# Kernel optimization log

Hardware: AMD Instinct MI355X
Metric: run time of the kernel (lower is better)

## Reference

```python
import jax, jax.numpy as jnp
import numpy as np

B, T, D, H, C = 128, 512, 128, 64, 45

def _p(key, shape, scale):
    return jax.random.normal(key, shape, dtype=jnp.float32) * scale

def setup_inputs() -> dict:
    key = jax.random.key(0)
    ks = jax.random.split(key, 10)
    sD, sH, s2H = 1.0 / np.sqrt(D), 1.0 / np.sqrt(H), 1.0 / np.sqrt(2 * H)
    b = jnp.zeros((4 * H,), jnp.float32)
    return {
        "x": jax.random.normal(ks[0], (B, T, D), dtype=jnp.float32),
        "W1f": _p(ks[1], (D, 4 * H), sD), "U1f": _p(ks[2], (H, 4 * H), sH), "b1f": b,
        "W1b": _p(ks[3], (D, 4 * H), sD), "U1b": _p(ks[4], (H, 4 * H), sH), "b1b": b,
        "W2f": _p(ks[5], (2 * H, 4 * H), s2H), "U2f": _p(ks[6], (H, 4 * H), sH), "b2f": b,
        "W2b": _p(ks[7], (2 * H, 4 * H), s2H), "U2b": _p(ks[8], (H, 4 * H), sH), "b2b": b,
        "Wd": _p(ks[9], (2 * H, C), s2H), "bd": jnp.zeros((C,), jnp.float32),
    }

def _lstm_dir(x, W, U, b, reverse):
    # Keras LSTM with activation=relu, recurrent_activation=sigmoid, gate order [i,f,c,o].
    if reverse:
        x = x[:, ::-1, :]
    xz = jnp.einsum('btd,dg->btg', x, W) + b  # precompute input projections [B,T,4H]
    h0 = jnp.zeros((x.shape[0], H), x.dtype)

    def step(carry, z_t):
        h, c = carry
        z = z_t + h @ U  # [B,4H]
        i, f, g, o = jnp.split(z, 4, axis=-1)
        c = jax.nn.sigmoid(f) * c + jax.nn.sigmoid(i) * jax.nn.relu(g)
        h = jax.nn.sigmoid(o) * jax.nn.relu(c)
        return (h, c), h

    _, hs = jax.lax.scan(step, (h0, h0), jnp.swapaxes(xz, 0, 1))  # [T,B,H]
    hs = jnp.swapaxes(hs, 0, 1)  # [B,T,H]
    return hs[:, ::-1, :] if reverse else hs

def reference(x, W1f, U1f, b1f, W1b, U1b, b1b, W2f, U2f, b2f, W2b, U2b, b2b, Wd, bd):
    h1 = jnp.concatenate([_lstm_dir(x, W1f, U1f, b1f, False),
                          _lstm_dir(x, W1b, U1b, b1b, True)], axis=-1)   # [B,T,2H]
    h2 = jnp.concatenate([_lstm_dir(h1, W2f, U2f, b2f, False),
                          _lstm_dir(h1, W2b, U2b, b2b, True)], axis=-1)  # [B,T,2H]
    logits = h2 @ Wd + bd  # [B,T,C]
    return jax.nn.softmax(logits, axis=-1)
```

## Files before the change

### kernel.cpp

```cpp
#include <hip/hip_runtime.h>

#define TT 512
#define NB 128
#define DD 128
#define HH 64
#define CC 45

__device__ __forceinline__ float sigf(float x) { return 1.0f / (1.0f + __expf(-x)); }

#define LDS_BAR() asm volatile("s_waitcnt lgkmcnt(0)\n\ts_barrier" ::: "memory")

#define QP_XOR1(x) __int_as_float(__builtin_amdgcn_mov_dpp(__float_as_int(x), 0xB1, 0xF, 0xF, true))
#define QP_XOR2(x) __int_as_float(__builtin_amdgcn_mov_dpp(__float_as_int(x), 0x4E, 0xF, 0xF, true))

__global__ __launch_bounds__(256) void gemm_xz(
    const float* __restrict__ A, const float* __restrict__ Wf,
    const float* __restrict__ Wb, const float* __restrict__ biasf,
    const float* __restrict__ biasb, float* __restrict__ Cout)
{
    __shared__ float As[32][132];
    __shared__ float Bs[32][132];
    const int tid = threadIdx.x;
    const int m0 = blockIdx.x * 128;
    const int n0 = blockIdx.y * 128;
    const float* W   = (n0 < 256) ? Wf : Wb;
    const float* bia = (n0 < 256) ? biasf : biasb;
    const int nc0 = n0 & 255;

    const int ty = tid >> 4, tx = tid & 15;
    const int arow = tid >> 3, akv = (tid & 7) << 2;
    const int bkr  = tid >> 5, bnv = (tid & 31) << 2;

    float acc[8][8];
    #pragma unroll
    for (int i = 0; i < 8; ++i)
        #pragma unroll
        for (int j = 0; j < 8; ++j) acc[i][j] = 0.f;

    for (int k0 = 0; k0 < 128; k0 += 32) {
        #pragma unroll
        for (int rr = 0; rr < 4; ++rr) {
            const int r = arow + rr * 32;
            const float4 av = *(const float4*)&A[(size_t)(m0 + r) * 128 + k0 + akv];
            As[akv + 0][r] = av.x; As[akv + 1][r] = av.y;
            As[akv + 2][r] = av.z; As[akv + 3][r] = av.w;
        }
        #pragma unroll
        for (int rr = 0; rr < 4; ++rr) {
            const int kr = bkr + rr * 8;
            *(float4*)&Bs[kr][bnv] =
                *(const float4*)&W[(size_t)(k0 + kr) * 256 + nc0 + bnv];
        }
        __syncthreads();
        #pragma unroll
        for (int k = 0; k < 32; ++k) {
            float av[8], bv[8];
            *(float4*)&av[0] = *(const float4*)&As[k][ty * 8];
            *(float4*)&av[4] = *(const float4*)&As[k][ty * 8 + 4];
            *(float4*)&bv[0] = *(const float4*)&Bs[k][tx * 8];
            *(float4*)&bv[4] = *(const float4*)&Bs[k][tx * 8 + 4];
            #pragma unroll
            for (int i = 0; i < 8; ++i)
                #pragma unroll
                for (int j = 0; j < 8; ++j)
                    acc[i][j] = __fmaf_rn(av[i], bv[j], acc[i][j]);
        }
        __syncthreads();
    }
    #pragma unroll
    for (int i = 0; i < 8; ++i) {
        const size_t rbase = (size_t)(m0 + ty * 8 + i) * 512 + n0 + tx * 8;
        float4 o;
        o.x = acc[i][0] + bia[nc0 + tx * 8 + 0];
        o.y = acc[i][1] + bia[nc0 + tx * 8 + 1];
        o.z = acc[i][2] + bia[nc0 + tx * 8 + 2];
        o.w = acc[i][3] + bia[nc0 + tx * 8 + 3];
        *(float4*)&Cout[rbase] = o;
        o.x = acc[i][4] + bia[nc0 + tx * 8 + 4];
        o.y = acc[i][5] + bia[nc0 + tx * 8 + 5];
        o.z = acc[i][6] + bia[nc0 + tx * 8 + 6];
        o.w = acc[i][7] + bia[nc0 + tx * 8 + 7];
        *(float4*)&Cout[rbase + 4] = o;
    }
}

__global__
__attribute__((amdgpu_flat_work_group_size(512, 512), amdgpu_waves_per_eu(1, 2)))
void lstm_rec_qp(
    const float* __restrict__ xz, const float* __restrict__ Uf,
    const float* __restrict__ Ubw, float* __restrict__ hout)
{
    const int b   = blockIdx.x & 127;
    const int dir = blockIdx.x >> 7;
    const int tid = threadIdx.x;
    const int w    = tid >> 6;
    const int lane = tid & 63;
    const int gate = lane & 3;
    const int colL = (lane >> 2) & 7;
    const int kh   = lane >> 5;
    const int col  = w * 8 + colL;
    const int gcol = gate * 64 + col;
    const float* U = dir ? Ubw : Uf;

    __shared__ float hbuf[2][64];

    const float* Ug = U + (size_t)(kh * 32) * 256 + gcol;
    float u0  = Ug[ 0*256], u1  = Ug[ 1*256], u2  = Ug[ 2*256], u3  = Ug[ 3*256];
    float u4  = Ug[ 4*256], u5  = Ug[ 5*256], u6  = Ug[ 6*256], u7  = Ug[ 7*256];
    float u8  = Ug[ 8*256], u9  = Ug[ 9*256], u10 = Ug[10*256], u11 = Ug[11*256];
    float u12 = Ug[12*256], u13 = Ug[13*256], u14 = Ug[14*256], u15 = Ug[15*256];
    float u16 = Ug[16*256], u17 = Ug[17*256], u18 = Ug[18*256], u19 = Ug[19*256];
    float u20 = Ug[20*256], u21 = Ug[21*256], u22 = Ug[22*256], u23 = Ug[23*256];
    float u24 = Ug[24*256], u25 = Ug[25*256], u26 = Ug[26*256], u27 = Ug[27*256];
    float u28 = Ug[28*256], u29 = Ug[29*256], u30 = Ug[30*256], u31 = Ug[31*256];
    asm volatile("" : "+v"(u0),"+v"(u1),"+v"(u2),"+v"(u3),
                      "+v"(u4),"+v"(u5),"+v"(u6),"+v"(u7));
    asm volatile("" : "+v"(u8),"+v"(u9),"+v"(u10),"+v"(u11),
                      "+v"(u12),"+v"(u13),"+v"(u14),"+v"(u15));
    asm volatile("" : "+v"(u16),"+v"(u17),"+v"(u18),"+v"(u19),
                      "+v"(u20),"+v"(u21),"+v"(u22),"+v"(u23));
    asm volatile("" : "+v"(u24),"+v"(u25),"+v"(u26),"+v"(u27),
                      "+v"(u28),"+v"(u29),"+v"(u30),"+v"(u31));

    if (tid < 64) hbuf[0][tid] = 0.f;
    float c = 0.f;
    __syncthreads();

    const float* xzb = xz + (size_t)b * TT * 512 + (size_t)dir * 256 + gcol;
    float*       hob = hout + (size_t)b * TT * 128 + (size_t)dir * 64 + col;

    int trow = dir ? (TT - 1) : 0;
    const int ts = dir ? -1 : 1;
    float xc = xzb[(size_t)trow * 512];
    float x1 = xzb[(size_t)(trow + ts) * 512];

    for (int s = 0; s < TT; ++s) {
        const int p = s & 1;
        float x2 = 0.f;
        if (s + 2 < TT) x2 = xzb[(size_t)(trow + 2 * ts) * 512];

        float a0 = 0.f, a1 = 0.f, a2 = 0.f, a3 = 0.f;
#define ACC(J, A,B,C,D) { const float4 hv = *(const float4*)&hbuf[p][kh*32 + 4*(J)]; \
        a0 = __fmaf_rn(hv.x, A, a0); a1 = __fmaf_rn(hv.y, B, a1); \
        a2 = __fmaf_rn(hv.z, C, a2); a3 = __fmaf_rn(hv.w, D, a3); }
        ACC(0,u0 ,u1 ,u2 ,u3 ) ACC(1,u4 ,u5 ,u6 ,u7 )
        ACC(2,u8 ,u9 ,u10,u11) ACC(3,u12,u13,u14,u15)
        ACC(4,u16,u17,u18,u19) ACC(5,u20,u21,u22,u23)
        ACC(6,u24,u25,u26,u27) ACC(7,u28,u29,u30,u31)
#undef ACC
        float part = (a0 + a1) + (a2 + a3);

        part += __shfl_xor(part, 32);
        const float z = xc + part;

        const float a = (gate == 2) ? fmaxf(z, 0.f) : sigf(z);

        const float b0 = QP_XOR1(a);
        const float b1 = QP_XOR2(a);
        const float b2 = QP_XOR2(b0);
        const float ai = (gate == 0) ? a : (gate == 1) ? b0 : (gate == 2) ? b1 : b2;
        const float af = (gate == 1) ? a : (gate == 0) ? b0 : (gate == 3) ? b1 : b2;
        const float ag = (gate == 2) ? a : (gate == 3) ? b0 : (gate == 0) ? b1 : b2;
        const float ao = (gate == 3) ? a : (gate == 2) ? b0 : (gate == 1) ? b1 : b2;

        c = af * c + ai * ag;
        const float h = ao * fmaxf(c, 0.f);

        if ((lane & 0x23) == 0) {
            hbuf[p ^ 1][col] = h;
            hob[(size_t)trow * 128] = h;
        }

        LDS_BAR();

        xc = x1; x1 = x2;
        trow += ts;
    }
}

__global__ __launch_bounds__(256) void dense_softmax(
    const float* __restrict__ h2, const float* __restrict__ Wd,
    const float* __restrict__ bd, float* __restrict__ out)
{
    __shared__ float Wl[128 * 45];
    __shared__ float bl[48];
    __shared__ float hrow[4][128];
    const int tid = threadIdx.x;
    for (int i = tid; i < 128 * 45; i += 256) Wl[i] = Wd[i];
    if (tid < 45) bl[tid] = bd[tid];
    __syncthreads();

    const int w = tid >> 6, l = tid & 63;
    const size_t row0 = (size_t)blockIdx.x * 64;
    for (int rr = 0; rr < 16; ++rr) {
        const size_t m = row0 + (size_t)rr * 4 + w;
        const float2 hv = *(const float2*)&h2[m * 128 + l * 2];
        hrow[w][l * 2] = hv.x;
        hrow[w][l * 2 + 1] = hv.y;
        __syncthreads();
        float lg = -3.0e38f;
        if (l < CC) {
            lg = bl[l];
            #pragma unroll 8
            for (int k = 0; k < 128; ++k) lg = __fmaf_rn(hrow[w][k], Wl[k * 45 + l], lg);
        }
        float mx = lg;
        #pragma unroll
        for (int off = 32; off >= 1; off >>= 1) mx = fmaxf(mx, __shfl_xor(mx, off));
        const float e = (l < CC) ? __expf(lg - mx) : 0.f;
        float sm = e;
        #pragma unroll
        for (int off = 32; off >= 1; off >>= 1) sm += __shfl_xor(sm, off);
        if (l < CC) out[m * 45 + l] = e / sm;
        __syncthreads();
    }
}

extern "C" void kernel_launch(void* const* d_in, const int* in_sizes, int n_in,
                              void* d_out, int out_size, void* d_ws, size_t ws_size,
                              hipStream_t stream)
{
    const float* x   = (const float*)d_in[0];
    const float* W1f = (const float*)d_in[1];
    const float* U1f = (const float*)d_in[2];
    const float* b1f = (const float*)d_in[3];
    const float* W1b = (const float*)d_in[4];
    const float* U1b = (const float*)d_in[5];
    const float* b1b = (const float*)d_in[6];
    const float* W2f = (const float*)d_in[7];
    const float* U2f = (const float*)d_in[8];
    const float* b2f = (const float*)d_in[9];
    const float* W2b = (const float*)d_in[10];
    const float* U2b = (const float*)d_in[11];
    const float* b2b = (const float*)d_in[12];
    const float* Wd  = (const float*)d_in[13];
    const float* bd  = (const float*)d_in[14];

    float* xz = (float*)d_ws;
    float* h  = (float*)((char*)d_ws + (size_t)65536 * 512 * 4);

    const dim3 gemm_grid(512, 4);
    const dim3 rec_grid(256);
    const dim3 dense_grid(1024);

    gemm_xz<<<gemm_grid, dim3(256), 0, stream>>>(x, W1f, W1b, b1f, b1b, xz);
    lstm_rec_qp<<<rec_grid, dim3(512), 0, stream>>>(xz, U1f, U1b, h);
    gemm_xz<<<gemm_grid, dim3(256), 0, stream>>>(h, W2f, W2b, b2f, b2b, xz);
    lstm_rec_qp<<<rec_grid, dim3(512), 0, stream>>>(xz, U2f, U2b, h);
    dense_softmax<<<dense_grid, dim3(256), 0, stream>>>(h, Wd, bd, (float*)d_out);
}
```

Baseline: 710.3 us.

## Use split-bf16 MFMA for input projection GEMM

Replaces the FP32 FMA tiled GEMM for the input projections with a kernel on bf16 MFMA instructions. Each operand is split into high and low bf16 parts and three MFMAs per tile (hh, hl, lh) approximate FP32 accuracy. The whole K=128 is staged in LDS at once, and the grid is reordered so adjacent blocks share the same A rows. The aim is to cut GEMM time, at the cost of per-element conversion work, more LDS use, and scalar (non-vectorised) output stores.

```diff
diff --git a/kernel.cpp b/kernel.cpp
--- a/kernel.cpp
+++ b/kernel.cpp
@@ -13,74 +13,97 @@
 #define QP_XOR1(x) __int_as_float(__builtin_amdgcn_mov_dpp(__float_as_int(x), 0xB1, 0xF, 0xF, true))
 #define QP_XOR2(x) __int_as_float(__builtin_amdgcn_mov_dpp(__float_as_int(x), 0x4E, 0xF, 0xF, true))
 
-__global__ __launch_bounds__(256) void gemm_xz(
+__device__ __forceinline__ ushort f2bf(float x) {
+    uint u = __float_as_uint(x);
+    u += 0x7FFFu + ((u >> 16) & 1u);
+    return (ushort)(u >> 16);
+}
+__device__ __forceinline__ float bf2f(ushort h) { return __uint_as_float(((uint)h) << 16); }
+
+typedef short short8 __attribute__((ext_vector_type(8)));
+typedef float f32x4 __attribute__((ext_vector_type(4)));
+
+__global__ __launch_bounds__(256, 1) void gemm_xz_mfma(
     const float* __restrict__ A, const float* __restrict__ Wf,
     const float* __restrict__ Wb, const float* __restrict__ biasf,
     const float* __restrict__ biasb, float* __restrict__ Cout)
 {
-    __shared__ float As[32][132];
-    __shared__ float Bs[32][132];
+    __shared__ ushort Ah[128][136];
+    __shared__ ushort Al[128][136];
+    __shared__ ushort Wh[128][136];
+    __shared__ ushort Wl[128][136];
+
     const int tid = threadIdx.x;
-    const int m0 = blockIdx.x * 128;
-    const int n0 = blockIdx.y * 128;
+    const int n0  = blockIdx.x * 128;
+    const int m0  = blockIdx.y * 128;
     const float* W   = (n0 < 256) ? Wf : Wb;
     const float* bia = (n0 < 256) ? biasf : biasb;
     const int nc0 = n0 & 255;
 
-    const int ty = tid >> 4, tx = tid & 15;
-    const int arow = tid >> 3, akv = (tid & 7) << 2;
-    const int bkr  = tid >> 5, bnv = (tid & 31) << 2;
-
-    float acc[8][8];
+    {
+        const int r  = tid >> 1;
+        const int cb = (tid & 1) * 64;
+        #pragma unroll
+        for (int i = 0; i < 16; ++i) {
+            const int c = cb + i * 4;
+            const float4 v = *(const float4*)&A[(size_t)(m0 + r) * 128 + c];
+            const ushort hx = f2bf(v.x), hy = f2bf(v.y), hz = f2bf(v.z), hw = f2bf(v.w);
+            const ushort lx = f2bf(v.x - bf2f(hx)), ly = f2bf(v.y - bf2f(hy));
+            const ushort lz = f2bf(v.z - bf2f(hz)), lw = f2bf(v.w - bf2f(hw));
+            *(uint*)&Ah[r][c]     = (uint)hx | ((uint)hy << 16);
+            *(uint*)&Ah[r][c + 2] = (uint)hz | ((uint)hw << 16);
+            *(uint*)&Al[r][c]     = (uint)lx | ((uint)ly << 16);
+            *(uint*)&Al[r][c + 2] = (uint)lz | ((uint)lw << 16);
+            const float4 wv = *(const float4*)&W[(size_t)r * 256 + nc0 + c];
+            const ushort whx = f2bf(wv.x), why = f2bf(wv.y), whz = f2bf(wv.z), whw = f2bf(wv.w);
+            Wh[c + 0][r] = whx; Wl[c + 0][r] = f2bf(wv.x - bf2f(whx));
+            Wh[c + 1][r] = why; Wl[c + 1][r] = f2bf(wv.y - bf2f(why));
+            Wh[c + 2][r] = whz; Wl[c + 2][r] = f2bf(wv.z - bf2f(whz));
+            Wh[c + 3][r] = whw; Wl[c + 3][r] = f2bf(wv.w - bf2f(whw));
+        }
+    }
+    __syncthreads();
+
+    const int lane = tid & 63, wv_ = tid >> 6;
+    const int fr = lane & 15, fg = lane >> 4;
+
+    f32x4 acc[2][8];
     #pragma unroll
-    for (int i = 0; i < 8; ++i)
-        #pragma unroll
-        for (int j = 0; j < 8; ++j) acc[i][j] = 0.f;
-
-    for (int k0 = 0; k0 < 128; k0 += 32) {
-        #pragma unroll
-        for (int rr = 0; rr < 4; ++rr) {
-            const int r = arow + rr * 32;
-            const float4 av = *(const float4*)&A[(size_t)(m0 + r) * 128 + k0 + akv];
-            As[akv + 0][r] = av.x; As[akv + 1][r] = av.y;
-            As[akv + 2][r] = av.z; As[akv + 3][r] = av.w;
-        }
-        #pragma unroll
-        for (int rr = 0; rr < 4; ++rr) {
-            const int kr = bkr + rr * 8;
-            *(float4*)&Bs[kr][bnv] =
-                *(const float4*)&W[(size_t)(k0 + kr) * 256 + nc0 + bnv];
-        }
-        __syncthreads();
-        #pragma unroll
-        for (int k = 0; k < 32; ++k) {
-            float av[8], bv[8];
-            *(float4*)&av[0] = *(const float4*)&As[k][ty * 8];
-            *(float4*)&av[4] = *(const float4*)&As[k][ty * 8 + 4];
-            *(float4*)&bv[0] = *(const float4*)&Bs[k][tx * 8];
-            *(float4*)&bv[4] = *(const float4*)&Bs[k][tx * 8 + 4];
+    for (int ms = 0; ms < 2; ++ms)
+        #pragma unroll
+        for (int nt = 0; nt < 8; ++nt) acc[ms][nt] = (f32x4){0.f, 0.f, 0.f, 0.f};
+
+    #pragma unroll
+    for (int ks = 0; ks < 4; ++ks) {
+        const int kb = ks * 32 + fg * 8;
+        const short8 ah0 = *(const short8*)&Ah[wv_ * 32 + fr][kb];
+        const short8 al0 = *(const short8*)&Al[wv_ * 32 + fr][kb];
+        const short8 ah1 = *(const short8*)&Ah[wv_ * 32 + 16 + fr][kb];
+        const short8 al1 = *(const short8*)&Al[wv_ * 32 + 16 + fr][kb];
+        #pragma unroll
+        for (int nt = 0; nt < 8; ++nt) {
+            const short8 bh = *(const short8*)&Wh[nt * 16 + fr][kb];
+            const short8 bl = *(const short8*)&Wl[nt * 16 + fr][kb];
+            acc[0][nt] = __builtin_amdgcn_mfma_f32_16x16x32_bf16(ah0, bh, acc[0][nt], 0, 0, 0);
+            acc[0][nt] = __builtin_amdgcn_mfma_f32_16x16x32_bf16(ah0, bl, acc[0][nt], 0, 0, 0);
+            acc[0][nt] = __builtin_amdgcn_mfma_f32_16x16x32_bf16(al0, bh, acc[0][nt], 0, 0, 0);
+            acc[1][nt] = __builtin_amdgcn_mfma_f32_16x16x32_bf16(ah1, bh, acc[1][nt], 0, 0, 0);
+            acc[1][nt] = __builtin_amdgcn_mfma_f32_16x16x32_bf16(ah1, bl, acc[1][nt], 0, 0, 0);
+            acc[1][nt] = __builtin_amdgcn_mfma_f32_16x16x32_bf16(al1, bh, acc[1][nt], 0, 0, 0);
+        }
+    }
+
+    #pragma unroll
+    for (int nt = 0; nt < 8; ++nt) {
+        const float bb = bia[nc0 + nt * 16 + fr];
+        #pragma unroll
+        for (int ms = 0; ms < 2; ++ms) {
             #pragma unroll
-            for (int i = 0; i < 8; ++i)
-                #pragma unroll
-                for (int j = 0; j < 8; ++j)
-                    acc[i][j] = __fmaf_rn(av[i], bv[j], acc[i][j]);
-        }
-        __syncthreads();
-    }
-    #pragma unroll
-    for (int i = 0; i < 8; ++i) {
-        const size_t rbase = (size_t)(m0 + ty * 8 + i) * 512 + n0 + tx * 8;
-        float4 o;
-        o.x = acc[i][0] + bia[nc0 + tx * 8 + 0];
-        o.y = acc[i][1] + bia[nc0 + tx * 8 + 1];
-        o.z = acc[i][2] + bia[nc0 + tx * 8 + 2];
-        o.w = acc[i][3] + bia[nc0 + tx * 8 + 3];
-        *(float4*)&Cout[rbase] = o;
-        o.x = acc[i][4] + bia[nc0 + tx * 8 + 4];
-        o.y = acc[i][5] + bia[nc0 + tx * 8 + 5];
-        o.z = acc[i][6] + bia[nc0 + tx * 8 + 6];
-        o.w = acc[i][7] + bia[nc0 + tx * 8 + 7];
-        *(float4*)&Cout[rbase + 4] = o;
+            for (int j = 0; j < 4; ++j) {
+                const int mg = m0 + wv_ * 32 + ms * 16 + fg * 4 + j;
+                Cout[(size_t)mg * 512 + n0 + nt * 16 + fr] = acc[ms][nt][j] + bb;
+            }
+        }
     }
 }
 
@@ -239,13 +262,13 @@
     float* xz = (float*)d_ws;
     float* h  = (float*)((char*)d_ws + (size_t)65536 * 512 * 4);
 
-    const dim3 gemm_grid(512, 4);
+    const dim3 gemm_grid(4, 512);
     const dim3 rec_grid(256);
     const dim3 dense_grid(1024);
 
-    gemm_xz<<<gemm_grid, dim3(256), 0, stream>>>(x, W1f, W1b, b1f, b1b, xz);
+    gemm_xz_mfma<<<gemm_grid, dim3(256), 0, stream>>>(x, W1f, W1b, b1f, b1b, xz);
     lstm_rec_qp<<<rec_grid, dim3(512), 0, stream>>>(xz, U1f, U1b, h);
-    gemm_xz<<<gemm_grid, dim3(256), 0, stream>>>(h, W2f, W2b, b2f, b2b, xz);
+    gemm_xz_mfma<<<gemm_grid, dim3(256), 0, stream>>>(h, W2f, W2b, b2f, b2b, xz);
     lstm_rec_qp<<<rec_grid, dim3(512), 0, stream>>>(xz, U2f, U2b, h);
     dense_softmax<<<dense_grid, dim3(256), 0, stream>>>(h, Wd, bd, (float*)d_out);
 }
```

New measurement: 649.8 us. 8.5% less time.
